# Optimization experiments

Hardware: AMD Instinct MI355X
Metric: run time of the kernel (lower is better)

The kernel has to match this reference:

```python
import jax, jax.numpy as jnp
import numpy as np

B, N, S, I, W, D, Z = 2, 25, 4096, 63, 256, 8, 16


def setup_inputs() -> dict:
    key = jax.random.key(0)
    ks = jax.random.split(key, 7)
    k_in = np.sqrt(1.0 / I)
    k_w = np.sqrt(1.0 / W)
    x = jax.random.normal(ks[0], (B, N, S, I), dtype=jnp.float32)
    W0 = jax.random.uniform(ks[1], (N, I, W), minval=-k_in, maxval=k_in, dtype=jnp.float32)
    b0 = jax.random.uniform(ks[2], (N, W), minval=-k_in, maxval=k_in, dtype=jnp.float32)
    Wmid = jax.random.uniform(ks[3], (D - 2, N, W, W), minval=-k_w, maxval=k_w, dtype=jnp.float32)
    bmid = jax.random.uniform(ks[4], (D - 2, N, W), minval=-k_w, maxval=k_w, dtype=jnp.float32)
    Wlast = jax.random.uniform(ks[5], (N, W, Z), minval=-k_w, maxval=k_w, dtype=jnp.float32)
    blast = jax.random.uniform(ks[6], (N, Z), minval=-k_w, maxval=k_w, dtype=jnp.float32)
    return {"x": x, "W0": W0, "b0": b0, "Wmid": Wmid, "bmid": bmid, "Wlast": Wlast, "blast": blast}


def reference(x, W0, b0, Wmid, bmid, Wlast, blast):
    # layer 0: [B,N,S,I] x [N,I,W] -> [B,N,S,W], ReLU
    h = jax.nn.relu(jnp.einsum('bnsi,niw->bnsw', x, W0) + b0[None, :, None, :])

    # middle D-2 layers, weights broadcast across batch (no materialized copies)
    def step(h, wb):
        w, b = wb  # w: [N,W,W], b: [N,W]
        h = jax.nn.relu(jnp.einsum('bnsw,nwv->bnsv', h, w) + b[None, :, None, :])
        return h, None

    h, _ = jax.lax.scan(step, h, (Wmid, bmid))

    # last layer: no activation
    out = jnp.einsum('bnsw,nwz->bnsz', h, Wlast) + blast[None, :, None, :]
    return out  # [B,N,S,Z]
```

## Files before the change

kernel.cpp:

```cpp
#include <hip/hip_runtime.h>
#include <stdint.h>

#define B_ 2
#define N_ 25
#define S_ 4096
#define I_ 63
#define W_ 256
#define D_ 8
#define Z_ 16

typedef float f32x4 __attribute__((ext_vector_type(4)));
typedef __bf16 bf16x8 __attribute__((ext_vector_type(8)));

__device__ __forceinline__ unsigned short f2bf(float x) {
  unsigned int u = __float_as_uint(x);
  unsigned int r = (u + 0x7fffu + ((u >> 16) & 1u)) >> 16;
  return (unsigned short)r;
}
__device__ __forceinline__ float bf2f(unsigned short h) {
  return __uint_as_float(((unsigned int)h) << 16);
}

__global__ void prep_tr(const float* __restrict__ in,
                        unsigned short* __restrict__ oh,
                        unsigned short* __restrict__ ol,
                        int K, int V, int Kp, int tiles_k, int tiles_v) {
  __shared__ float tile[64][65];
  int tpm = tiles_k * tiles_v;
  int m  = blockIdx.x / tpm;
  int tt = blockIdx.x - m * tpm;
  int tk = tt / tiles_v, tv = tt - tk * tiles_v;
  int k0 = tk * 64, v0 = tv * 64;
  const float* src = in + (size_t)m * K * V;
  int c  = threadIdx.x & 63;
  int r0 = threadIdx.x >> 6;
#pragma unroll
  for (int i = 0; i < 16; ++i) {
    int r = i * 4 + r0;
    int k = k0 + r, v = v0 + c;
    tile[r][c] = (k < K && v < V) ? src[(size_t)k * V + v] : 0.0f;
  }
  __syncthreads();
  unsigned short* dh = oh + (size_t)m * V * Kp;
  unsigned short* dl = ol + (size_t)m * V * Kp;
#pragma unroll
  for (int i = 0; i < 16; ++i) {
    int r = i * 4 + r0;
    int v = v0 + r, k = k0 + c;
    if (v < V && k < Kp) {
      float val = tile[c][r];
      unsigned short hi = f2bf(val);
      unsigned short lo = f2bf(val - bf2f(hi));
      dh[(size_t)v * Kp + k] = hi;
      dl[(size_t)v * Kp + k] = lo;
    }
  }
}

__device__ __forceinline__ void stage_B(const unsigned short* __restrict__ w,
                                        int rowlen, int kbase,
                                        unsigned short* Bb, int tid) {
  int wavebase = (tid >> 6) << 6;
#pragma unroll
  for (int p = 0; p < 2; ++p) {
    int t = tid + p * 512;
    int v = t >> 2, blkp = t & 3;
    int blk = blkp ^ ((v >> 1) & 3);
    const unsigned short* g = w + (size_t)v * rowlen + kbase + blk * 8;
    unsigned short* ldsb = Bb + (size_t)(wavebase + p * 512) * 8;
    __builtin_amdgcn_global_load_lds((const __attribute__((address_space(1))) void*)g,
                                     (__attribute__((address_space(3))) void*)ldsb,
                                     16, 0, 0);
  }
}

__global__ __launch_bounds__(512) void mlp_fused(
    const float* __restrict__ x, const float* __restrict__ b0,
    const float* __restrict__ bmid, const float* __restrict__ blast,
    const unsigned short* __restrict__ wt0h, const unsigned short* __restrict__ wt0l,
    const unsigned short* __restrict__ wtmh, const unsigned short* __restrict__ wtml,
    const unsigned short* __restrict__ wtlh, const unsigned short* __restrict__ wtll,
    float* __restrict__ out) {
  extern __shared__ unsigned short smem[];
  unsigned short* Ah = smem;
  unsigned short* Al = smem + 32768;
  unsigned short* Bb = smem + 65536;

  const int tid  = threadIdx.x;
  const int lane = tid & 63;
  const int wave = tid >> 6;
  const int lrow = lane & 15;
  const int lk   = lane >> 4;

  const int g  = blockIdx.x;
  const int n  = g >> 6;
  const int t  = g & 63;
  const int bb = t >> 5;
  const int s0 = (t & 31) * 128;

  const int tg = wave >> 2;
  const int vg = wave & 3;

  {
    const float* xp = x + (((size_t)bb * N_ + n) * S_ + s0) * I_;
#pragma unroll
    for (int i = 0; i < 16; ++i) {
      int e = tid + i * 512;
      int tok = e >> 6, k = e & 63;
      float val = (k < I_) ? xp[tok * I_ + k] : 0.0f;
      unsigned short hi = f2bf(val);
      unsigned short lo = f2bf(val - bf2f(hi));
      int off = tok * 256 + ((((k >> 3) ^ (tok & 31)) << 3) | (k & 7));
      Ah[off] = hi;
      Al[off] = lo;
    }
  }
  __syncthreads();

  f32x4 acc[4][4];

#pragma unroll 1
  for (int l = 0; l < 7; ++l) {
    const unsigned short *wh, *wl;
    const float* bias;
    int rowlen, nkc;
    if (l == 0) {
      wh = wt0h + (size_t)n * (W_ * 64);
      wl = wt0l + (size_t)n * (W_ * 64);
      bias = b0 + n * W_;
      rowlen = 64; nkc = 2;
    } else {
      size_t o = ((size_t)(l - 1) * N_ + n) * ((size_t)W_ * W_);
      wh = wtmh + o;
      wl = wtml + o;
      bias = bmid + ((size_t)(l - 1) * N_ + n) * W_;
      rowlen = W_; nkc = 8;
    }
#pragma unroll
    for (int i = 0; i < 4; ++i)
#pragma unroll
      for (int j = 0; j < 4; ++j)
        acc[i][j] = (f32x4){0.f, 0.f, 0.f, 0.f};

#pragma unroll 1
    for (int kc = 0; kc < nkc; ++kc) {
      stage_B(wh, rowlen, kc * 32, Bb, tid);
      asm volatile("s_waitcnt vmcnt(0)" ::: "memory");
      __syncthreads();

      bf16x8 ahf[4], alf[4];
#pragma unroll
      for (int rt = 0; rt < 4; ++rt) {
        int tok = tg * 64 + rt * 16 + lrow;
        int off = tok * 256 + (((kc * 4 + lk) ^ (tok & 31)) << 3);
        ahf[rt] = *(const bf16x8*)(Ah + off);
        alf[rt] = *(const bf16x8*)(Al + off);
      }
#pragma unroll
      for (int vt = 0; vt < 4; ++vt) {
        int v = vg * 64 + vt * 16 + lrow;
        bf16x8 bf = *(const bf16x8*)(Bb + v * 32 + ((lk ^ ((v >> 1) & 3)) << 3));
#pragma unroll
        for (int rt = 0; rt < 4; ++rt)
          acc[rt][vt] = __builtin_amdgcn_mfma_f32_16x16x32_bf16(ahf[rt], bf, acc[rt][vt], 0, 0, 0);
#pragma unroll
        for (int rt = 0; rt < 4; ++rt)
          acc[rt][vt] = __builtin_amdgcn_mfma_f32_16x16x32_bf16(alf[rt], bf, acc[rt][vt], 0, 0, 0);
      }
      __syncthreads();

      stage_B(wl, rowlen, kc * 32, Bb, tid);
      asm volatile("s_waitcnt vmcnt(0)" ::: "memory");
      __syncthreads();
#pragma unroll
      for (int vt = 0; vt < 4; ++vt) {
        int v = vg * 64 + vt * 16 + lrow;
        bf16x8 bf = *(const bf16x8*)(Bb + v * 32 + ((lk ^ ((v >> 1) & 3)) << 3));
#pragma unroll
        for (int rt = 0; rt < 4; ++rt)
          acc[rt][vt] = __builtin_amdgcn_mfma_f32_16x16x32_bf16(ahf[rt], bf, acc[rt][vt], 0, 0, 0);
      }
      __syncthreads();
    }

#pragma unroll
    for (int vt = 0; vt < 4; ++vt) {
      int col = vg * 64 + vt * 16 + lrow;
      float bv = bias[col];
#pragma unroll
      for (int rt = 0; rt < 4; ++rt) {
        f32x4 cfr = acc[rt][vt];
#pragma unroll
        for (int r = 0; r < 4; ++r) {
          int tok = tg * 64 + rt * 16 + lk * 4 + r;
          float val = fmaxf(cfr[r] + bv, 0.0f);
          unsigned short hi = f2bf(val);
          unsigned short lo = f2bf(val - bf2f(hi));
          int off = tok * 256 + ((((col >> 3) ^ (tok & 31)) << 3) | (col & 7));
          Ah[off] = hi;
          Al[off] = lo;
        }
      }
    }
    __syncthreads();
  }

  {
    const unsigned short* wh = wtlh + (size_t)n * (Z_ * W_);
    const unsigned short* wl = wtll + (size_t)n * (Z_ * W_);
    f32x4 accL = (f32x4){0.f, 0.f, 0.f, 0.f};
#pragma unroll 1
    for (int kc = 0; kc < 8; ++kc) {
      if (wave == 0) {
        int v = lane >> 2, blkp = lane & 3;
        int blk = blkp ^ ((v >> 1) & 3);
        const unsigned short* gh = wh + v * W_ + kc * 32 + blk * 8;
        const unsigned short* gl = wl + v * W_ + kc * 32 + blk * 8;
        __builtin_amdgcn_global_load_lds((const __attribute__((address_space(1))) void*)gh,
                                         (__attribute__((address_space(3))) void*)Bb, 16, 0, 0);
        __builtin_amdgcn_global_load_lds((const __attribute__((address_space(1))) void*)gl,
                                         (__attribute__((address_space(3))) void*)(Bb + 512), 16, 0, 0);
      }
      asm volatile("s_waitcnt vmcnt(0)" ::: "memory");
      __syncthreads();
      int tok = wave * 16 + lrow;
      int aoff = tok * 256 + (((kc * 4 + lk) ^ (tok & 31)) << 3);
      bf16x8 ahf = *(const bf16x8*)(Ah + aoff);
      bf16x8 alf = *(const bf16x8*)(Al + aoff);
      int v = lrow;
      int boff = v * 32 + ((lk ^ ((v >> 1) & 3)) << 3);
      bf16x8 bh = *(const bf16x8*)(Bb + boff);
      bf16x8 bl = *(const bf16x8*)(Bb + 512 + boff);
      accL = __builtin_amdgcn_mfma_f32_16x16x32_bf16(ahf, bh, accL, 0, 0, 0);
      accL = __builtin_amdgcn_mfma_f32_16x16x32_bf16(alf, bh, accL, 0, 0, 0);
      accL = __builtin_amdgcn_mfma_f32_16x16x32_bf16(ahf, bl, accL, 0, 0, 0);
      __syncthreads();
    }
    float bv = blast[n * Z_ + lrow];
    float* op = out + (((size_t)bb * N_ + n) * S_ + s0) * Z_;
#pragma unroll
    for (int r = 0; r < 4; ++r) {
      int tok = wave * 16 + lk * 4 + r;
      op[(size_t)tok * Z_ + lrow] = accL[r] + bv;
    }
  }
}

__global__ __launch_bounds__(256) void mlp_fallback(
    const float* __restrict__ x, const float* __restrict__ W0,
    const float* __restrict__ b0, const float* __restrict__ Wmid,
    const float* __restrict__ bmid, const float* __restrict__ Wlast,
    const float* __restrict__ blast, float* __restrict__ out) {
  __shared__ float h[64][256];
  const int g  = blockIdx.x;
  const int n  = g >> 7;
  const int t  = g & 127;
  const int bb = t >> 6;
  const int s0 = (t & 63) * 64;
  const int v  = threadIdx.x;

  const float* xp = x + (((size_t)bb * N_ + n) * S_ + s0) * I_;
  float r[64];
  {
    const float* w = W0 + (size_t)n * I_ * W_;
    float bv = b0[n * W_ + v];
#pragma unroll 8
    for (int i = 0; i < 64; ++i) r[i] = bv;
    for (int k = 0; k < I_; ++k) {
      float wv = w[(size_t)k * W_ + v];
#pragma unroll
      for (int i = 0; i < 64; ++i) r[i] += xp[(size_t)i * I_ + k] * wv;
    }
#pragma unroll
    for (int i = 0; i < 64; ++i) h[i][v] = fmaxf(r[i], 0.f);
    __syncthreads();
  }
  for (int d = 0; d < D_ - 2; ++d) {
    const float* w = Wmid + ((size_t)d * N_ + n) * W_ * W_;
    float bv = bmid[((size_t)d * N_ + n) * W_ + v];
#pragma unroll 8
    for (int i = 0; i < 64; ++i) r[i] = bv;
    for (int k = 0; k < W_; ++k) {
      float wv = w[(size_t)k * W_ + v];
#pragma unroll
      for (int i = 0; i < 64; ++i) r[i] += h[i][k] * wv;
    }
    __syncthreads();
#pragma unroll
    for (int i = 0; i < 64; ++i) h[i][v] = fmaxf(r[i], 0.f);
    __syncthreads();
  }
  if (v < Z_) {
    const float* w = Wlast + (size_t)n * W_ * Z_;
    float bv = blast[n * Z_ + v];
#pragma unroll 8
    for (int i = 0; i < 64; ++i) r[i] = bv;
    for (int k = 0; k < W_; ++k) {
      float wv = w[(size_t)k * Z_ + v];
#pragma unroll
      for (int i = 0; i < 64; ++i) r[i] += h[i][k] * wv;
    }
    float* op = out + (((size_t)bb * N_ + n) * S_ + s0) * Z_;
#pragma unroll
    for (int i = 0; i < 64; ++i) op[(size_t)i * Z_ + v] = r[i];
  }
}

extern "C" void kernel_launch(void* const* d_in, const int* in_sizes, int n_in,
                              void* d_out, int out_size, void* d_ws, size_t ws_size,
                              hipStream_t stream) {
  const float* x     = (const float*)d_in[0];
  const float* W0    = (const float*)d_in[1];
  const float* b0    = (const float*)d_in[2];
  const float* Wmid  = (const float*)d_in[3];
  const float* bmid  = (const float*)d_in[4];
  const float* Wlast = (const float*)d_in[5];
  const float* blast = (const float*)d_in[6];
  float* out = (float*)d_out;
  (void)in_sizes; (void)n_in; (void)out_size;

  const size_t n_wt0 = (size_t)N_ * W_ * 64;
  const size_t n_wtm = (size_t)(D_ - 2) * N_ * W_ * W_;
  const size_t n_wtl = (size_t)N_ * Z_ * W_;
  const size_t need_bytes = 2 * (n_wt0 + n_wtm + n_wtl) * sizeof(unsigned short);

  bool use_main = (ws_size >= need_bytes);
  if (use_main) {
    hipError_t e = hipFuncSetAttribute((const void*)mlp_fused,
                                       hipFuncAttributeMaxDynamicSharedMemorySize,
                                       147456);
    if (e != hipSuccess) use_main = false;
  }

  if (use_main) {
    unsigned short* ws   = (unsigned short*)d_ws;
    unsigned short* wt0h = ws;
    unsigned short* wt0l = wt0h + n_wt0;
    unsigned short* wtmh = wt0l + n_wt0;
    unsigned short* wtml = wtmh + n_wtm;
    unsigned short* wtlh = wtml + n_wtm;
    unsigned short* wtll = wtlh + n_wtl;

    prep_tr<<<25 * 4, 256, 0, stream>>>(W0, wt0h, wt0l, I_, W_, 64, 1, 4);
    prep_tr<<<150 * 16, 256, 0, stream>>>(Wmid, wtmh, wtml, W_, W_, W_, 4, 4);
    prep_tr<<<25 * 4, 256, 0, stream>>>(Wlast, wtlh, wtll, W_, Z_, W_, 4, 1);

    mlp_fused<<<1600, 512, 147456, stream>>>(x, b0, bmid, blast,
                                             wt0h, wt0l, wtmh, wtml, wtlh, wtll, out);
  } else {
    mlp_fallback<<<25 * 128, 256, 0, stream>>>(x, W0, b0, Wmid, bmid, Wlast, blast, out);
  }
}
```

Baseline: 906.0 us.

## Load weights directly to registers with double buffering, halve token tile, remap blocks

Drops the LDS staging of weight tiles and the barriers around it. Each wave now loads its B fragments straight from global memory into registers, with double buffering across K chunks. The token tile per block shrinks from 128 to 64, which roughly halves LDS use, so occupancy can rise (launch bounds ask for 4 blocks per CU). Block IDs are remapped so that neighbouring blocks work on different networks. The trade-off is more global and L2 traffic for weights, since waves no longer share one staged tile.

```diff
diff --git a/kernel.cpp b/kernel.cpp
--- a/kernel.cpp
+++ b/kernel.cpp
@@ -57,55 +57,35 @@
   }
 }
 
-__device__ __forceinline__ void stage_B(const unsigned short* __restrict__ w,
-                                        int rowlen, int kbase,
-                                        unsigned short* Bb, int tid) {
-  int wavebase = (tid >> 6) << 6;
-#pragma unroll
-  for (int p = 0; p < 2; ++p) {
-    int t = tid + p * 512;
-    int v = t >> 2, blkp = t & 3;
-    int blk = blkp ^ ((v >> 1) & 3);
-    const unsigned short* g = w + (size_t)v * rowlen + kbase + blk * 8;
-    unsigned short* ldsb = Bb + (size_t)(wavebase + p * 512) * 8;
-    __builtin_amdgcn_global_load_lds((const __attribute__((address_space(1))) void*)g,
-                                     (__attribute__((address_space(3))) void*)ldsb,
-                                     16, 0, 0);
-  }
-}
-
-__global__ __launch_bounds__(512) void mlp_fused(
+__global__ __launch_bounds__(512, 4) void mlp_fused(
     const float* __restrict__ x, const float* __restrict__ b0,
     const float* __restrict__ bmid, const float* __restrict__ blast,
     const unsigned short* __restrict__ wt0h, const unsigned short* __restrict__ wt0l,
     const unsigned short* __restrict__ wtmh, const unsigned short* __restrict__ wtml,
     const unsigned short* __restrict__ wtlh, const unsigned short* __restrict__ wtll,
     float* __restrict__ out) {
-  extern __shared__ unsigned short smem[];
-  unsigned short* Ah = smem;
-  unsigned short* Al = smem + 32768;
-  unsigned short* Bb = smem + 65536;
+  __shared__ unsigned short Ah[64 * 256];
+  __shared__ unsigned short Al[64 * 256];
 
   const int tid  = threadIdx.x;
   const int lane = tid & 63;
   const int wave = tid >> 6;
   const int lrow = lane & 15;
   const int lk   = lane >> 4;
-
-  const int g  = blockIdx.x;
-  const int n  = g >> 6;
-  const int t  = g & 63;
-  const int bb = t >> 5;
-  const int s0 = (t & 31) * 128;
-
-  const int tg = wave >> 2;
-  const int vg = wave & 3;
+  const int koff = lk * 8;
+
+  const int bid = blockIdx.x;
+  const int w   = (bid & 7) * 400 + (bid >> 3);
+  const int n   = w >> 7;
+  const int t   = w & 127;
+  const int bb  = t >> 6;
+  const int s0  = (t & 63) * 64;
 
   {
     const float* xp = x + (((size_t)bb * N_ + n) * S_ + s0) * I_;
 #pragma unroll
-    for (int i = 0; i < 16; ++i) {
-      int e = tid + i * 512;
+    for (int i = 0; i < 8; ++i) {
+      int e = i * 512 + tid;
       int tok = e >> 6, k = e & 63;
       float val = (k < I_) ? xp[tok * I_ + k] : 0.0f;
       unsigned short hi = f2bf(val);
@@ -117,7 +97,8 @@
   }
   __syncthreads();
 
-  f32x4 acc[4][4];
+  const int cbase = wave * 32 + lrow;
+  f32x4 acc[4][2];
 
 #pragma unroll 1
   for (int l = 0; l < 7; ++l) {
@@ -139,60 +120,57 @@
 #pragma unroll
     for (int i = 0; i < 4; ++i)
 #pragma unroll
-      for (int j = 0; j < 4; ++j)
+      for (int j = 0; j < 2; ++j)
         acc[i][j] = (f32x4){0.f, 0.f, 0.f, 0.f};
 
-#pragma unroll 1
-    for (int kc = 0; kc < nkc; ++kc) {
-      stage_B(wh, rowlen, kc * 32, Bb, tid);
-      asm volatile("s_waitcnt vmcnt(0)" ::: "memory");
-      __syncthreads();
-
+    auto loadB = [&](bf16x8 (&dst)[2][2], int kc) {
+#pragma unroll
+      for (int vt = 0; vt < 2; ++vt) {
+        size_t ro = (size_t)(cbase + vt * 16) * rowlen + kc * 32 + koff;
+        dst[vt][0] = *(const bf16x8*)(wh + ro);
+        dst[vt][1] = *(const bf16x8*)(wl + ro);
+      }
+    };
+    auto stepK = [&](bf16x8 (&buf)[2][2], int kc) {
       bf16x8 ahf[4], alf[4];
 #pragma unroll
       for (int rt = 0; rt < 4; ++rt) {
-        int tok = tg * 64 + rt * 16 + lrow;
+        int tok = rt * 16 + lrow;
         int off = tok * 256 + (((kc * 4 + lk) ^ (tok & 31)) << 3);
         ahf[rt] = *(const bf16x8*)(Ah + off);
         alf[rt] = *(const bf16x8*)(Al + off);
       }
 #pragma unroll
-      for (int vt = 0; vt < 4; ++vt) {
-        int v = vg * 64 + vt * 16 + lrow;
-        bf16x8 bf = *(const bf16x8*)(Bb + v * 32 + ((lk ^ ((v >> 1) & 3)) << 3));
-#pragma unroll
-        for (int rt = 0; rt < 4; ++rt)
-          acc[rt][vt] = __builtin_amdgcn_mfma_f32_16x16x32_bf16(ahf[rt], bf, acc[rt][vt], 0, 0, 0);
-#pragma unroll
-        for (int rt = 0; rt < 4; ++rt)
-          acc[rt][vt] = __builtin_amdgcn_mfma_f32_16x16x32_bf16(alf[rt], bf, acc[rt][vt], 0, 0, 0);
-      }
-      __syncthreads();
-
-      stage_B(wl, rowlen, kc * 32, Bb, tid);
-      asm volatile("s_waitcnt vmcnt(0)" ::: "memory");
-      __syncthreads();
-#pragma unroll
-      for (int vt = 0; vt < 4; ++vt) {
-        int v = vg * 64 + vt * 16 + lrow;
-        bf16x8 bf = *(const bf16x8*)(Bb + v * 32 + ((lk ^ ((v >> 1) & 3)) << 3));
-#pragma unroll
-        for (int rt = 0; rt < 4; ++rt)
-          acc[rt][vt] = __builtin_amdgcn_mfma_f32_16x16x32_bf16(ahf[rt], bf, acc[rt][vt], 0, 0, 0);
-      }
-      __syncthreads();
-    }
-
-#pragma unroll
-    for (int vt = 0; vt < 4; ++vt) {
-      int col = vg * 64 + vt * 16 + lrow;
+      for (int vt = 0; vt < 2; ++vt)
+#pragma unroll
+        for (int rt = 0; rt < 4; ++rt) {
+          acc[rt][vt] = __builtin_amdgcn_mfma_f32_16x16x32_bf16(ahf[rt], buf[vt][0], acc[rt][vt], 0, 0, 0);
+          acc[rt][vt] = __builtin_amdgcn_mfma_f32_16x16x32_bf16(alf[rt], buf[vt][0], acc[rt][vt], 0, 0, 0);
+          acc[rt][vt] = __builtin_amdgcn_mfma_f32_16x16x32_bf16(ahf[rt], buf[vt][1], acc[rt][vt], 0, 0, 0);
+        }
+    };
+
+    bf16x8 bufA[2][2], bufB[2][2];
+    loadB(bufA, 0);
+#pragma unroll 1
+    for (int kc = 0; kc < nkc; kc += 2) {
+      if (kc + 1 < nkc) loadB(bufB, kc + 1);
+      stepK(bufA, kc);
+      if (kc + 2 < nkc) loadB(bufA, kc + 2);
+      if (kc + 1 < nkc) stepK(bufB, kc + 1);
+    }
+
+    __syncthreads();
+#pragma unroll
+    for (int vt = 0; vt < 2; ++vt) {
+      int col = wave * 32 + vt * 16 + lrow;
       float bv = bias[col];
 #pragma unroll
       for (int rt = 0; rt < 4; ++rt) {
         f32x4 cfr = acc[rt][vt];
 #pragma unroll
         for (int r = 0; r < 4; ++r) {
-          int tok = tg * 64 + rt * 16 + lk * 4 + r;
+          int tok = rt * 16 + lk * 4 + r;
           float val = fmaxf(cfr[r] + bv, 0.0f);
           unsigned short hi = f2bf(val);
           unsigned short lo = f2bf(val - bf2f(hi));
@@ -205,42 +183,29 @@
     __syncthreads();
   }
 
-  {
+  if (wave < 4) {
     const unsigned short* wh = wtlh + (size_t)n * (Z_ * W_);
     const unsigned short* wl = wtll + (size_t)n * (Z_ * W_);
+    const int rt = wave;
     f32x4 accL = (f32x4){0.f, 0.f, 0.f, 0.f};
-#pragma unroll 1
+#pragma unroll
     for (int kc = 0; kc < 8; ++kc) {
-      if (wave == 0) {
-        int v = lane >> 2, blkp = lane & 3;
-        int blk = blkp ^ ((v >> 1) & 3);
-        const unsigned short* gh = wh + v * W_ + kc * 32 + blk * 8;
-        const unsigned short* gl = wl + v * W_ + kc * 32 + blk * 8;
-        __builtin_amdgcn_global_load_lds((const __attribute__((address_space(1))) void*)gh,
-                                         (__attribute__((address_space(3))) void*)Bb, 16, 0, 0);
-        __builtin_amdgcn_global_load_lds((const __attribute__((address_space(1))) void*)gl,
-                                         (__attribute__((address_space(3))) void*)(Bb + 512), 16, 0, 0);
-      }
-      asm volatile("s_waitcnt vmcnt(0)" ::: "memory");
-      __syncthreads();
-      int tok = wave * 16 + lrow;
+      size_t ro = (size_t)lrow * W_ + kc * 32 + koff;
+      bf16x8 bh = *(const bf16x8*)(wh + ro);
+      bf16x8 bl = *(const bf16x8*)(wl + ro);
+      int tok = rt * 16 + lrow;
       int aoff = tok * 256 + (((kc * 4 + lk) ^ (tok & 31)) << 3);
       bf16x8 ahf = *(const bf16x8*)(Ah + aoff);
       bf16x8 alf = *(const bf16x8*)(Al + aoff);
-      int v = lrow;
-      int boff = v * 32 + ((lk ^ ((v >> 1) & 3)) << 3);
-      bf16x8 bh = *(const bf16x8*)(Bb + boff);
-      bf16x8 bl = *(const bf16x8*)(Bb + 512 + boff);
       accL = __builtin_amdgcn_mfma_f32_16x16x32_bf16(ahf, bh, accL, 0, 0, 0);
       accL = __builtin_amdgcn_mfma_f32_16x16x32_bf16(alf, bh, accL, 0, 0, 0);
       accL = __builtin_amdgcn_mfma_f32_16x16x32_bf16(ahf, bl, accL, 0, 0, 0);
-      __syncthreads();
     }
     float bv = blast[n * Z_ + lrow];
     float* op = out + (((size_t)bb * N_ + n) * S_ + s0) * Z_;
 #pragma unroll
     for (int r = 0; r < 4; ++r) {
-      int tok = wave * 16 + lk * 4 + r;
+      int tok = rt * 16 + lk * 4 + r;
       op[(size_t)tok * Z_ + lrow] = accL[r] + bv;
     }
   }
@@ -324,15 +289,7 @@
   const size_t n_wtl = (size_t)N_ * Z_ * W_;
   const size_t need_bytes = 2 * (n_wt0 + n_wtm + n_wtl) * sizeof(unsigned short);
 
-  bool use_main = (ws_size >= need_bytes);
-  if (use_main) {
-    hipError_t e = hipFuncSetAttribute((const void*)mlp_fused,
-                                       hipFuncAttributeMaxDynamicSharedMemorySize,
-                                       147456);
-    if (e != hipSuccess) use_main = false;
-  }
-
-  if (use_main) {
+  if (ws_size >= need_bytes) {
     unsigned short* ws   = (unsigned short*)d_ws;
     unsigned short* wt0h = ws;
     unsigned short* wt0l = wt0h + n_wt0;
@@ -345,8 +302,8 @@
     prep_tr<<<150 * 16, 256, 0, stream>>>(Wmid, wtmh, wtml, W_, W_, W_, 4, 4);
     prep_tr<<<25 * 4, 256, 0, stream>>>(Wlast, wtlh, wtll, W_, Z_, W_, 4, 1);
 
-    mlp_fused<<<1600, 512, 147456, stream>>>(x, b0, bmid, blast,
-                                             wt0h, wt0l, wtmh, wtml, wtlh, wtll, out);
+    mlp_fused<<<3200, 512, 0, stream>>>(x, b0, bmid, blast,
+                                        wt0h, wt0l, wtmh, wtml, wtlh, wtll, out);
   } else {
     mlp_fallback<<<25 * 128, 256, 0, stream>>>(x, W0, b0, Wmid, bmid, Wlast, blast, out);
   }
```

Measured after the change: 1.040 ms. 1.15x slower.

## Double-buffer weight tiles in LDS, remap block order, preload last-layer weights

Applied to the files above, without the earlier changes.

Weight staging becomes a double-buffered pipeline over hi/lo phases. The next B tile is loaded into a second LDS buffer while MFMAs run on the current one, with a partial vmcnt wait in place of a full drain. Blocks are remapped so consecutive block IDs are spread across 8 groups, and the last-layer weights are loaded in one shot by all waves, which removes the per-k syncs. This raises LDS use to 160KB per block, and the partial-wait count must match the number of loads stage_B issues.

```diff
diff --git a/kernel.cpp b/kernel.cpp
--- a/kernel.cpp
+++ b/kernel.cpp
@@ -82,9 +82,10 @@
     const unsigned short* __restrict__ wtlh, const unsigned short* __restrict__ wtll,
     float* __restrict__ out) {
   extern __shared__ unsigned short smem[];
-  unsigned short* Ah = smem;
-  unsigned short* Al = smem + 32768;
-  unsigned short* Bb = smem + 65536;
+  unsigned short* Ah  = smem;
+  unsigned short* Al  = smem + 32768;
+  unsigned short* Bb0 = smem + 65536;
+  unsigned short* Bb1 = smem + 73728;
 
   const int tid  = threadIdx.x;
   const int lane = tid & 63;
@@ -92,11 +93,12 @@
   const int lrow = lane & 15;
   const int lk   = lane >> 4;
 
-  const int g  = blockIdx.x;
-  const int n  = g >> 6;
-  const int t  = g & 63;
-  const int bb = t >> 5;
-  const int s0 = (t & 31) * 128;
+  const int bid = blockIdx.x;
+  const int w   = (bid & 7) * 200 + (bid >> 3);
+  const int n   = w >> 6;
+  const int t   = w & 63;
+  const int bb  = t >> 5;
+  const int s0  = (t & 31) * 128;
 
   const int tg = wave >> 2;
   const int vg = wave & 3;
@@ -105,7 +107,7 @@
     const float* xp = x + (((size_t)bb * N_ + n) * S_ + s0) * I_;
 #pragma unroll
     for (int i = 0; i < 16; ++i) {
-      int e = tid + i * 512;
+      int e = i * 512 + tid;
       int tok = e >> 6, k = e & 63;
       float val = (k < I_) ? xp[tok * I_ + k] : 0.0f;
       unsigned short hi = f2bf(val);
@@ -123,18 +125,18 @@
   for (int l = 0; l < 7; ++l) {
     const unsigned short *wh, *wl;
     const float* bias;
-    int rowlen, nkc;
+    int rowlen, nph;
     if (l == 0) {
       wh = wt0h + (size_t)n * (W_ * 64);
       wl = wt0l + (size_t)n * (W_ * 64);
       bias = b0 + n * W_;
-      rowlen = 64; nkc = 2;
+      rowlen = 64; nph = 4;
     } else {
       size_t o = ((size_t)(l - 1) * N_ + n) * ((size_t)W_ * W_);
       wh = wtmh + o;
       wl = wtml + o;
       bias = bmid + ((size_t)(l - 1) * N_ + n) * W_;
-      rowlen = W_; nkc = 8;
+      rowlen = W_; nph = 16;
     }
 #pragma unroll
     for (int i = 0; i < 4; ++i)
@@ -142,43 +144,51 @@
       for (int j = 0; j < 4; ++j)
         acc[i][j] = (f32x4){0.f, 0.f, 0.f, 0.f};
 
+    stage_B(wh, rowlen, 0, Bb0, tid);
+
+    bf16x8 ahf[4], alf[4];
 #pragma unroll 1
-    for (int kc = 0; kc < nkc; ++kc) {
-      stage_B(wh, rowlen, kc * 32, Bb, tid);
-      asm volatile("s_waitcnt vmcnt(0)" ::: "memory");
-      __syncthreads();
-
-      bf16x8 ahf[4], alf[4];
-#pragma unroll
-      for (int rt = 0; rt < 4; ++rt) {
-        int tok = tg * 64 + rt * 16 + lrow;
-        int off = tok * 256 + (((kc * 4 + lk) ^ (tok & 31)) << 3);
-        ahf[rt] = *(const bf16x8*)(Ah + off);
-        alf[rt] = *(const bf16x8*)(Al + off);
-      }
-#pragma unroll
-      for (int vt = 0; vt < 4; ++vt) {
-        int v = vg * 64 + vt * 16 + lrow;
-        bf16x8 bf = *(const bf16x8*)(Bb + v * 32 + ((lk ^ ((v >> 1) & 3)) << 3));
-#pragma unroll
-        for (int rt = 0; rt < 4; ++rt)
-          acc[rt][vt] = __builtin_amdgcn_mfma_f32_16x16x32_bf16(ahf[rt], bf, acc[rt][vt], 0, 0, 0);
-#pragma unroll
-        for (int rt = 0; rt < 4; ++rt)
-          acc[rt][vt] = __builtin_amdgcn_mfma_f32_16x16x32_bf16(alf[rt], bf, acc[rt][vt], 0, 0, 0);
+    for (int s = 0; s < nph; ++s) {
+      unsigned short* cur = (s & 1) ? Bb1 : Bb0;
+      unsigned short* nxt = (s & 1) ? Bb0 : Bb1;
+      if (s + 1 < nph) {
+        const unsigned short* wsrc = ((s + 1) & 1) ? wl : wh;
+        stage_B(wsrc, rowlen, ((s + 1) >> 1) * 32, nxt, tid);
+        asm volatile("s_waitcnt vmcnt(2)" ::: "memory");
+      } else {
+        asm volatile("s_waitcnt vmcnt(0)" ::: "memory");
       }
       __syncthreads();
 
-      stage_B(wl, rowlen, kc * 32, Bb, tid);
-      asm volatile("s_waitcnt vmcnt(0)" ::: "memory");
-      __syncthreads();
-#pragma unroll
-      for (int vt = 0; vt < 4; ++vt) {
-        int v = vg * 64 + vt * 16 + lrow;
-        bf16x8 bf = *(const bf16x8*)(Bb + v * 32 + ((lk ^ ((v >> 1) & 3)) << 3));
-#pragma unroll
-        for (int rt = 0; rt < 4; ++rt)
-          acc[rt][vt] = __builtin_amdgcn_mfma_f32_16x16x32_bf16(ahf[rt], bf, acc[rt][vt], 0, 0, 0);
+      int kc = s >> 1;
+      if ((s & 1) == 0) {
+#pragma unroll
+        for (int rt = 0; rt < 4; ++rt) {
+          int tok = tg * 64 + rt * 16 + lrow;
+          int off = tok * 256 + (((kc * 4 + lk) ^ (tok & 31)) << 3);
+          ahf[rt] = *(const bf16x8*)(Ah + off);
+          alf[rt] = *(const bf16x8*)(Al + off);
+        }
+#pragma unroll
+        for (int vt = 0; vt < 4; ++vt) {
+          int v = vg * 64 + vt * 16 + lrow;
+          bf16x8 bf = *(const bf16x8*)(cur + v * 32 + ((lk ^ ((v >> 1) & 3)) << 3));
+#pragma unroll
+          for (int rt = 0; rt < 4; ++rt)
+            acc[rt][vt] = __builtin_amdgcn_mfma_f32_16x16x32_bf16(ahf[rt], bf, acc[rt][vt], 0, 0, 0);
+#pragma unroll
+          for (int rt = 0; rt < 4; ++rt)
+            acc[rt][vt] = __builtin_amdgcn_mfma_f32_16x16x32_bf16(alf[rt], bf, acc[rt][vt], 0, 0, 0);
+        }
+      } else {
+#pragma unroll
+        for (int vt = 0; vt < 4; ++vt) {
+          int v = vg * 64 + vt * 16 + lrow;
+          bf16x8 bf = *(const bf16x8*)(cur + v * 32 + ((lk ^ ((v >> 1) & 3)) << 3));
+#pragma unroll
+          for (int rt = 0; rt < 4; ++rt)
+            acc[rt][vt] = __builtin_amdgcn_mfma_f32_16x16x32_bf16(ahf[rt], bf, acc[rt][vt], 0, 0, 0);
+        }
       }
       __syncthreads();
     }
@@ -208,33 +218,38 @@
   {
     const unsigned short* wh = wtlh + (size_t)n * (Z_ * W_);
     const unsigned short* wl = wtll + (size_t)n * (Z_ * W_);
+    int wavebase = (tid >> 6) << 6;
+#pragma unroll
+    for (int p = 0; p < 2; ++p) {
+      int idx = p * 512 + tid;
+      int c = idx >> 6;
+      int bq = idx & 63;
+      int v = bq >> 2, blkp = bq & 3;
+      int blk = blkp ^ ((v >> 1) & 3);
+      int kc = c >> 1, hl = c & 1;
+      const unsigned short* g = (hl ? wl : wh) + (size_t)v * W_ + kc * 32 + blk * 8;
+      unsigned short* ldsb = Bb0 + (size_t)(wavebase + p * 512) * 8;
+      __builtin_amdgcn_global_load_lds((const __attribute__((address_space(1))) void*)g,
+                                       (__attribute__((address_space(3))) void*)ldsb,
+                                       16, 0, 0);
+    }
+    asm volatile("s_waitcnt vmcnt(0)" ::: "memory");
+    __syncthreads();
+
     f32x4 accL = (f32x4){0.f, 0.f, 0.f, 0.f};
-#pragma unroll 1
+    int v = lrow;
+    int boff = v * 32 + ((lk ^ ((v >> 1) & 3)) << 3);
+#pragma unroll
     for (int kc = 0; kc < 8; ++kc) {
-      if (wave == 0) {
-        int v = lane >> 2, blkp = lane & 3;
-        int blk = blkp ^ ((v >> 1) & 3);
-        const unsigned short* gh = wh + v * W_ + kc * 32 + blk * 8;
-        const unsigned short* gl = wl + v * W_ + kc * 32 + blk * 8;
-        __builtin_amdgcn_global_load_lds((const __attribute__((address_space(1))) void*)gh,
-                                         (__attribute__((address_space(3))) void*)Bb, 16, 0, 0);
-        __builtin_amdgcn_global_load_lds((const __attribute__((address_space(1))) void*)gl,
-                                         (__attribute__((address_space(3))) void*)(Bb + 512), 16, 0, 0);
-      }
-      asm volatile("s_waitcnt vmcnt(0)" ::: "memory");
-      __syncthreads();
       int tok = wave * 16 + lrow;
       int aoff = tok * 256 + (((kc * 4 + lk) ^ (tok & 31)) << 3);
       bf16x8 ahf = *(const bf16x8*)(Ah + aoff);
       bf16x8 alf = *(const bf16x8*)(Al + aoff);
-      int v = lrow;
-      int boff = v * 32 + ((lk ^ ((v >> 1) & 3)) << 3);
-      bf16x8 bh = *(const bf16x8*)(Bb + boff);
-      bf16x8 bl = *(const bf16x8*)(Bb + 512 + boff);
+      bf16x8 bh = *(const bf16x8*)(Bb0 + (kc * 2) * 512 + boff);
+      bf16x8 bl = *(const bf16x8*)(Bb0 + (kc * 2 + 1) * 512 + boff);
       accL = __builtin_amdgcn_mfma_f32_16x16x32_bf16(ahf, bh, accL, 0, 0, 0);
       accL = __builtin_amdgcn_mfma_f32_16x16x32_bf16(alf, bh, accL, 0, 0, 0);
       accL = __builtin_amdgcn_mfma_f32_16x16x32_bf16(ahf, bl, accL, 0, 0, 0);
-      __syncthreads();
     }
     float bv = blast[n * Z_ + lrow];
     float* op = out + (((size_t)bb * N_ + n) * S_ + s0) * Z_;
@@ -328,7 +343,7 @@
   if (use_main) {
     hipError_t e = hipFuncSetAttribute((const void*)mlp_fused,
                                        hipFuncAttributeMaxDynamicSharedMemorySize,
-                                       147456);
+                                       163840);
     if (e != hipSuccess) use_main = false;
   }
 
@@ -345,7 +360,7 @@
     prep_tr<<<150 * 16, 256, 0, stream>>>(Wmid, wtmh, wtml, W_, W_, W_, 4, 4);
     prep_tr<<<25 * 4, 256, 0, stream>>>(Wlast, wtlh, wtll, W_, Z_, W_, 4, 1);
 
-    mlp_fused<<<1600, 512, 147456, stream>>>(x, b0, bmid, blast,
+    mlp_fused<<<1600, 512, 163840, stream>>>(x, b0, bmid, blast,
                                              wt0h, wt0l, wtmh, wtml, wtlh, wtll, out);
   } else {
     mlp_fallback<<<25 * 128, 256, 0, stream>>>(x, W0, b0, Wmid, bmid, Wlast, blast, out);
```

Measured after the change: 1.191 ms. 1.31x slower.
